# Kernel tuning notes

Hardware: AMD Instinct MI355X
Metric: run time of the kernel (lower is better)

## Reference

```python
import jax, jax.numpy as jnp
import numpy as np

N, T, I, H = 64, 256, 512, 1024


def mish(x):
    return x * jnp.tanh(jax.nn.softplus(x))


def setup_inputs() -> dict:
    key = jax.random.key(0)
    ks = jax.random.split(key, 10)
    s_i = 1.0 / np.sqrt(I)
    s_h = 1.0 / np.sqrt(H)
    return {
        "x": jax.random.normal(ks[0], (N, T, I), dtype=jnp.float32),
        "is_init": jax.random.randint(ks[1], (N, T), 0, 2) > 0,
        "hx": jax.random.normal(ks[2], (N, T, H), dtype=jnp.float32),
        "cx": jax.random.normal(ks[3], (N, T, H), dtype=jnp.float32),
        "W_ih": jax.random.normal(ks[4], (4 * H, I), dtype=jnp.float32) * s_i,
        "W_hh": jax.random.normal(ks[5], (4 * H, H), dtype=jnp.float32) * s_h,
        "b_ih": jax.random.normal(ks[6], (4 * H,), dtype=jnp.float32) * s_h,
        "b_hh": jax.random.normal(ks[7], (4 * H,), dtype=jnp.float32) * s_h,
        "W_out": jax.random.normal(ks[8], (H, H), dtype=jnp.float32) * s_h,
        "b_out": jax.random.normal(ks[9], (H,), dtype=jnp.float32) * s_h,
    }


def reference(x, is_init, hx, cx, W_ih, W_hh, b_ih, b_hh, W_out, b_out):
    # recurrent_mode branch: scan LSTMCell over time with reset masking
    reset = 1.0 - is_init.astype(x.dtype)[..., None]          # [N,T,1]
    h0, c0 = hx[:, 0], cx[:, 0]                                # [N,H]

    def step(carry, inp):
        h, c = carry
        x_t, r_t = inp                                         # [N,I], [N,1]
        h = h * r_t
        c = c * r_t
        gates = x_t @ W_ih.T + b_ih + h @ W_hh.T + b_hh       # [N,4H]
        i_g, f_g, g_g, o_g = jnp.split(gates, 4, axis=-1)
        c = jax.nn.sigmoid(f_g) * c + jax.nn.sigmoid(i_g) * jnp.tanh(g_g)
        h = jax.nn.sigmoid(o_g) * jnp.tanh(c)
        return (h, c), h

    xs = (jnp.swapaxes(x, 0, 1), jnp.swapaxes(reset, 0, 1))    # time-major
    (h_f, c_f), hs = jax.lax.scan(step, (h0, c0), xs)
    hs = jnp.swapaxes(hs, 0, 1)                                # [N,T,H]
    out = mish(hs @ W_out.T + b_out)                           # Linear + Mish
    t = hs.shape[1]
    return (out,
            jnp.broadcast_to(h_f[:, None, :], (h_f.shape[0], t, h_f.shape[1])),
            jnp.broadcast_to(c_f[:, None, :], (c_f.shape[0], t, c_f.shape[1])))
```

## Files before the change

### kernel.cpp

```cpp
#include <hip/hip_runtime.h>
#include <math.h>

#define N_ 64
#define T_ 256
#define I_ 512
#define H_ 1024

typedef unsigned short u16;
typedef unsigned int u32;
typedef unsigned long long u64;
typedef short bf16x8 __attribute__((ext_vector_type(8)));
typedef float f32x4 __attribute__((ext_vector_type(4)));
typedef u16 u16x4 __attribute__((ext_vector_type(4)));

__device__ __forceinline__ u16 f2bf(float f) {
    union { float f; unsigned int u; } x; x.f = f;
    unsigned int r = (x.u + 0x7FFFu + ((x.u >> 16) & 1u)) >> 16;
    return (u16)r;
}
__device__ __forceinline__ float bf2f(u16 u) {
    union { unsigned int u; float f; } x; x.u = ((unsigned int)u) << 16;
    return x.f;
}
__device__ __forceinline__ float sigf(float v) {
    return 1.0f / (1.0f + __expf(-v));
}
__device__ __forceinline__ float tanhfast(float x) {
    float e = __expf(2.0f * x);
    return 1.0f - 2.0f / (e + 1.0f);
}

__device__ __forceinline__ void gload_lds16n(const void* g, void* l) {
    __builtin_amdgcn_global_load_lds(
        (__attribute__((address_space(1))) void*)(g),
        (__attribute__((address_space(3))) void*)(l), 16, 0, 0);
}

#define VMW(Ncnt) do { \
    asm volatile("s_waitcnt vmcnt(" #Ncnt ")" ::: "memory"); \
    __builtin_amdgcn_sched_barrier(0); } while (0)

__device__ __forceinline__ float* c_ptr(int n, int t, int j, float* cA, float* cB) {
    return (n < 32) ? (cA + (((size_t)(n * 256 + t)) << 10) + j)
                    : (cB + (((size_t)((n - 32) * 256 + t)) << 10) + j);
}


__global__ __launch_bounds__(256) void pack_weights(
    const float* __restrict__ W_ih, const float* __restrict__ W_hh,
    const float* __restrict__ b_ih, const float* __restrict__ b_hh,
    u16* __restrict__ Wp, float* __restrict__ bp)
{
    const int rp = blockIdx.x;
    const int j = rp >> 2, g = rp & 3;
    const int src = g * H_ + j;
    const float* wi = W_ih + (size_t)src * I_;
    const float* wh = W_hh + (size_t)src * H_;
    u16* dst = Wp + (size_t)rp * (I_ + H_);
    for (int k = threadIdx.x; k < I_; k += 256) dst[k] = f2bf(wi[k]);
    for (int k = threadIdx.x; k < H_; k += 256) dst[I_ + k] = f2bf(wh[k]);
    if (threadIdx.x == 0) bp[rp] = b_ih[src] + b_hh[src];
}

__global__ __launch_bounds__(256) void conv_x(
    const float* __restrict__ x, u16* __restrict__ x_tb)
{
    const int t = blockIdx.x, n = blockIdx.y;
    const float* s = x + ((size_t)n * T_ + t) * I_;
    u16* d = x_tb + ((size_t)t * N_ + n) * I_;
    for (int k = threadIdx.x; k < I_; k += 256) d[k] = f2bf(s[k]);
}

__global__ __launch_bounds__(256) void conv_wout(
    const float* __restrict__ W, u16* __restrict__ Wb)
{
    const size_t base = (size_t)blockIdx.x * 1024 + threadIdx.x;
    #pragma unroll
    for (int q = 0; q < 4; ++q) Wb[base + q * 256] = f2bf(W[base + q * 256]);
}

__global__ __launch_bounds__(256) void conv_hx(
    const float* __restrict__ hx, u16* __restrict__ hxbf)
{
    const int idx = blockIdx.x * 256 + threadIdx.x;
    const int n = idx >> 10, j = idx & (H_ - 1);
    hxbf[idx] = f2bf(hx[(size_t)n * T_ * H_ + j]);
}

__global__ __launch_bounds__(256) void prep_rel(
    const int* __restrict__ is_init, u16* __restrict__ rel16)
{
    __shared__ u16 ii[256];
    const int n = blockIdx.x, t = threadIdx.x;
    ii[t] = (u16)(is_init[n * T_ + t] != 0);
    __syncthreads();
    int rel = t + 1;
    for (int d = 0; d <= t; ++d) {
        if (ii[t - d]) { rel = d; break; }
    }
    rel16[n * T_ + t] = (u16)rel;
}

__global__ __launch_bounds__(256) void prep_bucket(
    const u16* __restrict__ rel16, u16* __restrict__ entries, u32* __restrict__ offs)
{
    __shared__ u32 hist[258];
    __shared__ u32 offsh[258];
    const int g = blockIdx.x, tid = threadIdx.x;
    for (int i = tid; i < 258; i += 256) hist[i] = 0;
    __syncthreads();
    for (int i = tid; i < 4096; i += 256) {
        const int n = g * 16 + (i & 15), t = i >> 4;
        atomicAdd(&hist[rel16[n * T_ + t]], 1u);
    }
    __syncthreads();
    if (tid == 0) {
        u32 acc = 0;
        for (int s = 0; s < 258; ++s) { offsh[s] = acc; acc += hist[s]; }
    }
    __syncthreads();
    for (int i = tid; i < 258; i += 256) {
        offs[g * 258 + i] = offsh[i];
        hist[i] = offsh[i];
    }
    __syncthreads();
    for (int i = tid; i < 4096; i += 256) {
        const int n = g * 16 + (i & 15), t = i >> 4;
        const int rel = rel16[n * T_ + t];
        const u32 slot = atomicAdd(&hist[rel], 1u);
        entries[g * 4096 + slot] = (u16)((t << 6) | n);
    }
}

__global__ __launch_bounds__(512) __attribute__((amdgpu_waves_per_eu(2, 2)))
void xgates_mfma(
    const u16* __restrict__ x_tb,
    const u16* __restrict__ Wp,
    const float* __restrict__ bp,
    u16* __restrict__ Xg)
{
    __shared__ u16 bls[2][8192];
    const int bx = blockIdx.x, by = blockIdx.y;
    const int tid = threadIdx.x;
    const int v = tid >> 6, l = tid & 63;
    const int l15 = l & 15, lh = l >> 4;
    const int rowb = bx * 256 + v * 32;
    const int colb = by * 256;

    const u16* ap0 = x_tb + (size_t)(rowb + l15) * I_ + lh * 8;
    const u16* ap1 = x_tb + (size_t)(rowb + 16 + l15) * I_ + lh * 8;
    const u16* bs0 = Wp + (size_t)(colb + (2 * v) * 16 + l15) * 1536 + lh * 8;
    const u16* bs1 = Wp + (size_t)(colb + (2 * v + 1) * 16 + l15) * 1536 + lh * 8;

    f32x4 acc[2][16];
    #pragma unroll
    for (int m = 0; m < 2; ++m)
        #pragma unroll
        for (int nt = 0; nt < 16; ++nt) acc[m][nt] = f32x4{0.f, 0.f, 0.f, 0.f};

#define STAGEX(S, B) do { \
    gload_lds16n(bs0 + (S) * 32, (char*)bls[B] + (2 * v) * 1024); \
    gload_lds16n(bs1 + (S) * 32, (char*)bls[B] + (2 * v + 1) * 1024); } while (0)

    STAGEX(0, 0);
    VMW(0); __syncthreads();
    int buf = 0;
    for (int s = 0; s < 16; ++s) {
        if (s < 15) STAGEX(s + 1, buf ^ 1);
        bf16x8 a0 = *(const bf16x8*)(ap0 + s * 32);
        bf16x8 a1 = *(const bf16x8*)(ap1 + s * 32);
        const char* bb = (const char*)bls[buf];
        #pragma unroll
        for (int nt = 0; nt < 16; ++nt) {
            bf16x8 bfr = *(const bf16x8*)(bb + nt * 1024 + l * 16);
            acc[0][nt] = __builtin_amdgcn_mfma_f32_16x16x32_bf16(a0, bfr, acc[0][nt], 0, 0, 0);
            acc[1][nt] = __builtin_amdgcn_mfma_f32_16x16x32_bf16(a1, bfr, acc[1][nt], 0, 0, 0);
        }
        VMW(0); __syncthreads();
        buf ^= 1;
    }
#undef STAGEX

    #pragma unroll
    for (int nt = 0; nt < 16; ++nt) {
        const int col = colb + nt * 16 + l15;
        const float bo = bp[col];
        #pragma unroll
        for (int mt = 0; mt < 2; ++mt)
            #pragma unroll
            for (int rg = 0; rg < 4; ++rg) {
                const int row = rowb + mt * 16 + lh * 4 + rg;
                Xg[(size_t)row * 4096 + col] = f2bf(acc[mt][nt][rg] + bo);
            }
    }
}

__global__ __launch_bounds__(256, 1) void lstm_seg(
    const u16* __restrict__ Xg,
    const u16* __restrict__ Wp,
    const float* __restrict__ cx,
    const u16* __restrict__ hxbf,
    const u16* __restrict__ entries,
    const u32* __restrict__ offs,
    u16* __restrict__ hs,
    float* __restrict__ cA,
    float* __restrict__ cB,
    float* __restrict__ c_final,
    u32* __restrict__ flags)
{
    __shared__ u16 wls[65536];
    const int tid = threadIdx.x;
    const int v = tid >> 6, l = tid & 63;
    const int l15 = l & 15, lh = l >> 4;
    const int u = blockIdx.x & 63, g = blockIdx.x >> 6;

    {
        const u16* src = Wp + (size_t)(u * 64 + v * 16 + l15) * 1536 + I_ + lh * 8;
        char* dst = (char*)wls + v * 32768;
        #pragma unroll
        for (int kk = 0; kk < 32; ++kk)
            gload_lds16n(src + kk * 32, dst + kk * 1024);
    }

    const u16* gent = entries + g * 4096;
    const u32* goff = offs + g * 258;
    u32* gflags = flags + g * 64 * 16;
    const char* wlsb = (const char*)wls;

    VMW(0);
    __syncthreads();

    {
        const int m0 = (int)goff[1];
        const int gtid = u * 256 + tid;
        for (int cell = gtid; cell < m0 * 512; cell += 64 * 256) {
            const int ri = cell >> 9, jj = cell & 511;
            const int j = jj * 2;
            const u16 e = gent[ri];
            const int t = e >> 6, n = e & 63;
            const u16* xp = Xg + ((size_t)t * 64 + n) * 4096 + 4 * j;
            const u16x4 xa = *(const u16x4*)(xp);
            const u16x4 xb = *(const u16x4*)(xp + 4);
            const float c0 = sigf(bf2f(xa[0])) * tanhfast(bf2f(xa[2]));
            const float h0 = sigf(bf2f(xa[3])) * tanhfast(c0);
            const float c1 = sigf(bf2f(xb[0])) * tanhfast(bf2f(xb[2]));
            const float h1 = sigf(bf2f(xb[3])) * tanhfast(c1);
            const size_t hrow = ((size_t)n * 256 + t) * 1024;
            __hip_atomic_store((u32*)(hs + hrow + j),
                               (u32)f2bf(h0) | ((u32)f2bf(h1) << 16),
                               __ATOMIC_RELAXED, __HIP_MEMORY_SCOPE_AGENT);
            __hip_atomic_store((u32*)c_ptr(n, t, j, cA, cB), __float_as_uint(c0),
                               __ATOMIC_RELAXED, __HIP_MEMORY_SCOPE_AGENT);
            __hip_atomic_store((u32*)c_ptr(n, t, j + 1, cA, cB), __float_as_uint(c1),
                               __ATOMIC_RELAXED, __HIP_MEMORY_SCOPE_AGENT);
            if (t == T_ - 1) {
                c_final[n * H_ + j] = c0;
                c_final[n * H_ + j + 1] = c1;
            }
        }
    }
    VMW(0);
    __syncthreads();
    if (tid == 0)
        __hip_atomic_store(gflags + u * 16, 1u,
                           __ATOMIC_RELAXED, __HIP_MEMORY_SCOPE_AGENT);
    if (tid < 64) {
        while (__hip_atomic_load(gflags + tid * 16, __ATOMIC_RELAXED,
                                 __HIP_MEMORY_SCOPE_AGENT) < 1u)
            __builtin_amdgcn_s_sleep(1);
    }
    __syncthreads();
    __builtin_amdgcn_sched_barrier(0);

    for (int s = 1; s <= 256; ++s) {
        if (goff[s] >= 4096u) break;
        const int base = (int)goff[s];
        const int last = (int)goff[s + 1] - 1;
        const int ntiles = ((last + 1 - base) + 15) >> 4;

        for (int mt = v; mt < ntiles; mt += 4) {
            const int ridx = base + mt * 16 + l15;
            const bool valid = (ridx <= last);
            const u16 e = gent[valid ? ridx : last];
            const int t = e >> 6, n = e & 63;

            const u16* rowsrc = (t == 0) ? (hxbf + n * 1024)
                               : (hs + ((size_t)n * 256 + (t - 1)) * 1024);
            const char* lsrc = (const char*)rowsrc + lh * 16;
            bf16x8 a[32];
            #pragma unroll
            for (int kk = 0; kk < 32; ++kk)
                a[kk] = *(const bf16x8*)(lsrc + kk * 64);

            const u16* xrow = Xg + ((size_t)t * 64 + n) * 4096;
            u16x4 xg[4]; float cprev[4];
            #pragma unroll
            for (int q = 0; q < 4; ++q) {
                const int jbq = u * 16 + q * 4 + lh;
                xg[q] = *(const u16x4*)(xrow + 4 * jbq);
                const float* cp = (t == 0) ? (cx + (size_t)n * T_ * H_ + jbq)
                                           : c_ptr(n, t - 1, jbq, cA, cB);
                cprev[q] = *cp;
            }

            f32x4 acc[4];
            #pragma unroll
            for (int q = 0; q < 4; ++q) acc[q] = f32x4{0.f, 0.f, 0.f, 0.f};
            #pragma unroll
            for (int q = 0; q < 4; ++q) {
                #pragma unroll
                for (int kk = 0; kk < 32; ++kk) {
                    bf16x8 wf = *(const bf16x8*)(wlsb + q * 32768 + kk * 1024 + l * 16);
                    acc[q] = __builtin_amdgcn_mfma_f32_16x16x32_bf16(wf, a[kk], acc[q], 0, 0, 0);
                }
            }

            #pragma unroll
            for (int q = 0; q < 4; ++q) {
                const int jbq = u * 16 + q * 4 + lh;
                const float ig = acc[q][0] + bf2f(xg[q][0]);
                const float fg = acc[q][1] + bf2f(xg[q][1]);
                const float gg = acc[q][2] + bf2f(xg[q][2]);
                const float og = acc[q][3] + bf2f(xg[q][3]);
                const float cn = sigf(fg) * cprev[q] + sigf(ig) * tanhfast(gg);
                const float hv = sigf(og) * tanhfast(cn);

                const float hvp = __shfl_down(hv, 16);
                if (valid && !(lh & 1)) {
                    __hip_atomic_store((u32*)(hs + ((size_t)n * 256 + t) * 1024 + jbq),
                                       (u32)f2bf(hv) | ((u32)f2bf(hvp) << 16),
                                       __ATOMIC_RELAXED, __HIP_MEMORY_SCOPE_AGENT);
                }
                if (valid) {
                    __hip_atomic_store((u32*)c_ptr(n, t, jbq, cA, cB),
                                       __float_as_uint(cn),
                                       __ATOMIC_RELAXED, __HIP_MEMORY_SCOPE_AGENT);
                    if (t == T_ - 1) c_final[n * H_ + jbq] = cn;
                }
            }
        }

        VMW(0);
        __syncthreads();
        if (tid == 0)
            __hip_atomic_store(gflags + u * 16, (u32)(s + 1),
                               __ATOMIC_RELAXED, __HIP_MEMORY_SCOPE_AGENT);
        if (tid < 64) {
            while (__hip_atomic_load(gflags + tid * 16, __ATOMIC_RELAXED,
                                     __HIP_MEMORY_SCOPE_AGENT) < (u32)(s + 1))
                __builtin_amdgcn_s_sleep(1);
        }
        __syncthreads();
        __builtin_amdgcn_sched_barrier(0);
    }
}

__global__ __launch_bounds__(512) __attribute__((amdgpu_waves_per_eu(2, 2)))
void out_proj_mfma(
    const u16* __restrict__ hs,
    const u16* __restrict__ Wo,
    const float* __restrict__ b_out,
    float* __restrict__ out0)
{
    __shared__ u16 bls[2][8192];
    const int bx = blockIdx.x, by = blockIdx.y;
    const int tid = threadIdx.x;
    const int v = tid >> 6, l = tid & 63;
    const int l15 = l & 15, lh = l >> 4;
    const int rowb = bx * 256 + v * 32;
    const int colb = by * 256;

    const u16* ap0 = hs + (size_t)(rowb + l15) * H_ + lh * 8;
    const u16* ap1 = hs + (size_t)(rowb + 16 + l15) * H_ + lh * 8;
    const u16* bs0 = Wo + (size_t)(colb + (2 * v) * 16 + l15) * H_ + lh * 8;
    const u16* bs1 = Wo + (size_t)(colb + (2 * v + 1) * 16 + l15) * H_ + lh * 8;

    f32x4 acc[2][16];
    #pragma unroll
    for (int m = 0; m < 2; ++m)
        #pragma unroll
        for (int nt = 0; nt < 16; ++nt) acc[m][nt] = f32x4{0.f, 0.f, 0.f, 0.f};

#define STAGEO(S, B) do { \
    gload_lds16n(bs0 + (S) * 32, (char*)bls[B] + (2 * v) * 1024); \
    gload_lds16n(bs1 + (S) * 32, (char*)bls[B] + (2 * v + 1) * 1024); } while (0)

    STAGEO(0, 0);
    VMW(0); __syncthreads();
    int buf = 0;
    for (int s = 0; s < 32; ++s) {
        if (s < 31) STAGEO(s + 1, buf ^ 1);
        bf16x8 a0 = *(const bf16x8*)(ap0 + s * 32);
        bf16x8 a1 = *(const bf16x8*)(ap1 + s * 32);
        const char* bb = (const char*)bls[buf];
        #pragma unroll
        for (int nt = 0; nt < 16; ++nt) {
            bf16x8 bfr = *(const bf16x8*)(bb + nt * 1024 + l * 16);
            acc[0][nt] = __builtin_amdgcn_mfma_f32_16x16x32_bf16(a0, bfr, acc[0][nt], 0, 0, 0);
            acc[1][nt] = __builtin_amdgcn_mfma_f32_16x16x32_bf16(a1, bfr, acc[1][nt], 0, 0, 0);
        }
        VMW(0); __syncthreads();
        buf ^= 1;
    }
#undef STAGEO

    #pragma unroll
    for (int nt = 0; nt < 16; ++nt) {
        const int col = colb + nt * 16 + l15;
        const float bo = b_out[col];
        #pragma unroll
        for (int mt = 0; mt < 2; ++mt)
            #pragma unroll
            for (int rg = 0; rg < 4; ++rg) {
                const int row = rowb + mt * 16 + lh * 4 + rg;
                const float y = acc[mt][nt][rg] + bo;
                const float sp = (y > 15.f) ? y : log1pf(__expf(y));
                out0[(size_t)row * H_ + col] = y * tanhfast(sp);
            }
    }
}

__global__ __launch_bounds__(256) void bcast_h(
    const u16* __restrict__ hs, float* __restrict__ out1)
{
    const size_t total = (size_t)N_ * T_ * H_;
    for (size_t idx = (size_t)blockIdx.x * 256 + threadIdx.x; idx < total;
         idx += (size_t)gridDim.x * 256) {
        const int n = (int)(idx >> 18);
        const int j = (int)(idx & (H_ - 1));
        out1[idx] = bf2f(hs[((size_t)n * T_ + (T_ - 1)) * H_ + j]);
    }
}

__global__ __launch_bounds__(256) void bcast_c(
    const float* __restrict__ c_final, float* __restrict__ out2)
{
    const size_t total = (size_t)N_ * T_ * H_;
    for (size_t idx = (size_t)blockIdx.x * 256 + threadIdx.x; idx < total;
         idx += (size_t)gridDim.x * 256) {
        const int n = (int)(idx >> 18);
        const int j = (int)(idx & (H_ - 1));
        out2[idx] = c_final[n * H_ + j];
    }
}

extern "C" void kernel_launch(void* const* d_in, const int* in_sizes, int n_in,
                              void* d_out, int out_size, void* d_ws, size_t ws_size,
                              hipStream_t stream) {
    const float* x      = (const float*)d_in[0];
    const int*   is_ini = (const int*)  d_in[1];
    const float* hx     = (const float*)d_in[2];
    const float* cx     = (const float*)d_in[3];
    const float* W_ih   = (const float*)d_in[4];
    const float* W_hh   = (const float*)d_in[5];
    const float* b_ih   = (const float*)d_in[6];
    const float* b_hh   = (const float*)d_in[7];
    const float* W_out  = (const float*)d_in[8];
    const float* b_out  = (const float*)d_in[9];

    float* out0 = (float*)d_out;
    float* out1 = out0 + (size_t)N_ * T_ * H_;
    float* out2 = out1 + (size_t)N_ * T_ * H_;

    char* ws = (char*)d_ws;
    u16*   x_tb    = (u16*)  (ws + 0);
    u16*   Wp      = (u16*)  (ws + 16777216);
    float* bp      = (float*)(ws + 29360128);
    u16*   Wo_b    = (u16*)  (ws + 29376512);
    float* c_final = (float*)(ws + 31473664);
    u16*   hxbf    = (u16*)  (ws + 31735808);
    u16*   rel16   = (u16*)  (ws + 31866880);
    u16*   entries = (u16*)  (ws + 31899648);
    u32*   offs    = (u32*)  (ws + 31932416);
    u32*   flags   = (u32*)  (ws + 31945472);
    float* cB      = (float*)(ws + 31961856);

    u16*   Xg = (u16*)out0;
    u16*   hs = (u16*)out2;
    float* cA = (float*)(out2 + (size_t)32 * 256 * 1024);

    hipMemsetAsync(flags, 0, 16384, stream);
    pack_weights<<<4096, 256, 0, stream>>>(W_ih, W_hh, b_ih, b_hh, Wp, bp);
    conv_x<<<dim3(T_, N_), 256, 0, stream>>>(x, x_tb);
    conv_wout<<<1024, 256, 0, stream>>>(W_out, Wo_b);
    conv_hx<<<256, 256, 0, stream>>>(hx, hxbf);
    prep_rel<<<64, 256, 0, stream>>>(is_ini, rel16);
    prep_bucket<<<4, 256, 0, stream>>>(rel16, entries, offs);

    xgates_mfma<<<dim3(64, 16), 512, 0, stream>>>(x_tb, Wp, bp, Xg);

    lstm_seg<<<256, 256, 0, stream>>>(Xg, Wp, cx, hxbf, entries, offs,
                                      hs, cA, cB, c_final, flags);

    out_proj_mfma<<<dim3(64, 4), 512, 0, stream>>>(hs, Wo_b, b_out, out0);
    bcast_h<<<2048, 256, 0, stream>>>(hs, out1);
    bcast_c<<<2048, 256, 0, stream>>>(c_final, out2);
}
```

Baseline: 1.067 ms.

## Permute gate rows for vectorized h/c stores and double-buffer tile loads

Reorders packed weight rows so that each lane owns four consecutive hidden units. This lets h be written as one 64-bit bf16x4 store and c as two 64-bit stores, with no cross-lane shuffle. The per-step tile loop is also software-pipelined with two register buffers, so the next tile's h-row, x-gate and c-prev loads are issued before the current tile's MFMAs. Risks are doubled register pressure from two 32-entry bf16x8 arrays, which could spill or reduce occupancy, and the need for the permutation to stay consistent with the Xg layout.

```diff
diff --git a/kernel.cpp b/kernel.cpp
--- a/kernel.cpp
+++ b/kernel.cpp
@@ -52,8 +52,10 @@
     u16* __restrict__ Wp, float* __restrict__ bp)
 {
     const int rp = blockIdx.x;
-    const int j = rp >> 2, g = rp & 3;
-    const int src = g * H_ + j;
+    const int g = rp & 3, jp = rp >> 2;
+    const int loc = jp & 15;
+    const int jsrc = (jp & ~15) + ((loc & 3) << 2) + (loc >> 2);
+    const int src = g * H_ + jsrc;
     const float* wi = W_ih + (size_t)src * I_;
     const float* wh = W_hh + (size_t)src * H_;
     u16* dst = Wp + (size_t)rp * (I_ + H_);
@@ -235,28 +237,26 @@
         const int gtid = u * 256 + tid;
         for (int cell = gtid; cell < m0 * 512; cell += 64 * 256) {
             const int ri = cell >> 9, jj = cell & 511;
-            const int j = jj * 2;
+            const int jt = jj * 2;
             const u16 e = gent[ri];
             const int t = e >> 6, n = e & 63;
-            const u16* xp = Xg + ((size_t)t * 64 + n) * 4096 + 4 * j;
-            const u16x4 xa = *(const u16x4*)(xp);
-            const u16x4 xb = *(const u16x4*)(xp + 4);
+            const int loc = jt & 15;
+            const int jp = (jt & ~15) + ((loc & 3) << 2) + (loc >> 2);
+            const u16* xrow = Xg + ((size_t)t * 64 + n) * 4096;
+            const u16x4 xa = *(const u16x4*)(xrow + 4 * jp);
+            const u16x4 xb = *(const u16x4*)(xrow + 4 * jp + 16);
             const float c0 = sigf(bf2f(xa[0])) * tanhfast(bf2f(xa[2]));
             const float h0 = sigf(bf2f(xa[3])) * tanhfast(c0);
             const float c1 = sigf(bf2f(xb[0])) * tanhfast(bf2f(xb[2]));
             const float h1 = sigf(bf2f(xb[3])) * tanhfast(c1);
             const size_t hrow = ((size_t)n * 256 + t) * 1024;
-            __hip_atomic_store((u32*)(hs + hrow + j),
+            __hip_atomic_store((u32*)(hs + hrow + jt),
                                (u32)f2bf(h0) | ((u32)f2bf(h1) << 16),
                                __ATOMIC_RELAXED, __HIP_MEMORY_SCOPE_AGENT);
-            __hip_atomic_store((u32*)c_ptr(n, t, j, cA, cB), __float_as_uint(c0),
+            const u64 cpk = (u64)__float_as_uint(c0) | ((u64)__float_as_uint(c1) << 32);
+            __hip_atomic_store((u64*)c_ptr(n, t, jt, cA, cB), cpk,
                                __ATOMIC_RELAXED, __HIP_MEMORY_SCOPE_AGENT);
-            __hip_atomic_store((u32*)c_ptr(n, t, j + 1, cA, cB), __float_as_uint(c1),
-                               __ATOMIC_RELAXED, __HIP_MEMORY_SCOPE_AGENT);
-            if (t == T_ - 1) {
-                c_final[n * H_ + j] = c0;
-                c_final[n * H_ + j + 1] = c1;
-            }
+            if (t == T_ - 1) *(float2*)(c_final + n * H_ + jt) = float2{c0, c1};
         }
     }
     VMW(0);
@@ -272,71 +272,91 @@
     __syncthreads();
     __builtin_amdgcn_sched_barrier(0);
 
+    bf16x8 Aa[32], Ba[32];
+    u16x4 Axg[4], Bxg[4];
+    float Acp[4], Bcp[4];
+    int At = 0, An = 0, Bt = 0, Bn = 0;
+    bool Av = false, Bv = false;
+
+#define LOADT(P, MT) do { \
+    const int ridx_ = base + (MT) * 16 + l15; \
+    P##v = (ridx_ <= last); \
+    const u16 e_ = gent[P##v ? ridx_ : last]; \
+    P##t = e_ >> 6; P##n = e_ & 63; \
+    const u16* rowsrc_ = (P##t == 0) ? (hxbf + P##n * 1024) \
+                       : (hs + ((size_t)P##n * 256 + (P##t - 1)) * 1024); \
+    const char* lsrc_ = (const char*)rowsrc_ + lh * 16; \
+    _Pragma("unroll") \
+    for (int kk_ = 0; kk_ < 32; ++kk_) \
+        P##a[kk_] = *(const bf16x8*)(lsrc_ + kk_ * 64); \
+    const u16* xrow_ = Xg + ((size_t)P##t * 64 + P##n) * 4096; \
+    _Pragma("unroll") \
+    for (int q_ = 0; q_ < 4; ++q_) { \
+        P##xg[q_] = *(const u16x4*)(xrow_ + 4 * (u * 16 + q_ * 4 + lh)); \
+        const int jt_ = u * 16 + lh * 4 + q_; \
+        P##cp[q_] = (P##t == 0) ? cx[(size_t)P##n * T_ * H_ + jt_] \
+                                : *c_ptr(P##n, P##t - 1, jt_, cA, cB); \
+    } \
+} while (0)
+
+#define PROCT(P) do { \
+    f32x4 acc_[4]; \
+    _Pragma("unroll") \
+    for (int q_ = 0; q_ < 4; ++q_) acc_[q_] = f32x4{0.f, 0.f, 0.f, 0.f}; \
+    _Pragma("unroll") \
+    for (int q_ = 0; q_ < 4; ++q_) { \
+        _Pragma("unroll") \
+        for (int kk_ = 0; kk_ < 32; ++kk_) { \
+            bf16x8 wf_ = *(const bf16x8*)(wlsb + q_ * 32768 + kk_ * 1024 + l * 16); \
+            acc_[q_] = __builtin_amdgcn_mfma_f32_16x16x32_bf16(wf_, P##a[kk_], acc_[q_], 0, 0, 0); \
+        } \
+    } \
+    float cn_[4], hv_[4]; \
+    _Pragma("unroll") \
+    for (int q_ = 0; q_ < 4; ++q_) { \
+        const float ig_ = acc_[q_][0] + bf2f(P##xg[q_][0]); \
+        const float fg_ = acc_[q_][1] + bf2f(P##xg[q_][1]); \
+        const float gg_ = acc_[q_][2] + bf2f(P##xg[q_][2]); \
+        const float og_ = acc_[q_][3] + bf2f(P##xg[q_][3]); \
+        cn_[q_] = sigf(fg_) * P##cp[q_] + sigf(ig_) * tanhfast(gg_); \
+        hv_[q_] = sigf(og_) * tanhfast(cn_[q_]); \
+    } \
+    if (P##v) { \
+        const int jt0_ = u * 16 + lh * 4; \
+        const u64 hp_ = (u64)f2bf(hv_[0]) | ((u64)f2bf(hv_[1]) << 16) \
+                      | ((u64)f2bf(hv_[2]) << 32) | ((u64)f2bf(hv_[3]) << 48); \
+        __hip_atomic_store((u64*)(hs + ((size_t)P##n * 256 + P##t) * 1024 + jt0_), \
+                           hp_, __ATOMIC_RELAXED, __HIP_MEMORY_SCOPE_AGENT); \
+        float* cp0_ = c_ptr(P##n, P##t, jt0_, cA, cB); \
+        const u64 c01_ = (u64)__float_as_uint(cn_[0]) | ((u64)__float_as_uint(cn_[1]) << 32); \
+        const u64 c23_ = (u64)__float_as_uint(cn_[2]) | ((u64)__float_as_uint(cn_[3]) << 32); \
+        __hip_atomic_store((u64*)cp0_, c01_, __ATOMIC_RELAXED, __HIP_MEMORY_SCOPE_AGENT); \
+        __hip_atomic_store((u64*)(cp0_ + 2), c23_, __ATOMIC_RELAXED, __HIP_MEMORY_SCOPE_AGENT); \
+        if (P##t == T_ - 1) \
+            *(float4*)(c_final + P##n * H_ + jt0_) = float4{cn_[0], cn_[1], cn_[2], cn_[3]}; \
+    } \
+} while (0)
+
     for (int s = 1; s <= 256; ++s) {
         if (goff[s] >= 4096u) break;
         const int base = (int)goff[s];
         const int last = (int)goff[s + 1] - 1;
         const int ntiles = ((last + 1 - base) + 15) >> 4;
 
-        for (int mt = v; mt < ntiles; mt += 4) {
-            const int ridx = base + mt * 16 + l15;
-            const bool valid = (ridx <= last);
-            const u16 e = gent[valid ? ridx : last];
-            const int t = e >> 6, n = e & 63;
-
-            const u16* rowsrc = (t == 0) ? (hxbf + n * 1024)
-                               : (hs + ((size_t)n * 256 + (t - 1)) * 1024);
-            const char* lsrc = (const char*)rowsrc + lh * 16;
-            bf16x8 a[32];
-            #pragma unroll
-            for (int kk = 0; kk < 32; ++kk)
-                a[kk] = *(const bf16x8*)(lsrc + kk * 64);
-
-            const u16* xrow = Xg + ((size_t)t * 64 + n) * 4096;
-            u16x4 xg[4]; float cprev[4];
-            #pragma unroll
-            for (int q = 0; q < 4; ++q) {
-                const int jbq = u * 16 + q * 4 + lh;
-                xg[q] = *(const u16x4*)(xrow + 4 * jbq);
-                const float* cp = (t == 0) ? (cx + (size_t)n * T_ * H_ + jbq)
-                                           : c_ptr(n, t - 1, jbq, cA, cB);
-                cprev[q] = *cp;
-            }
-
-            f32x4 acc[4];
-            #pragma unroll
-            for (int q = 0; q < 4; ++q) acc[q] = f32x4{0.f, 0.f, 0.f, 0.f};
-            #pragma unroll
-            for (int q = 0; q < 4; ++q) {
-                #pragma unroll
-                for (int kk = 0; kk < 32; ++kk) {
-                    bf16x8 wf = *(const bf16x8*)(wlsb + q * 32768 + kk * 1024 + l * 16);
-                    acc[q] = __builtin_amdgcn_mfma_f32_16x16x32_bf16(wf, a[kk], acc[q], 0, 0, 0);
-                }
-            }
-
-            #pragma unroll
-            for (int q = 0; q < 4; ++q) {
-                const int jbq = u * 16 + q * 4 + lh;
-                const float ig = acc[q][0] + bf2f(xg[q][0]);
-                const float fg = acc[q][1] + bf2f(xg[q][1]);
-                const float gg = acc[q][2] + bf2f(xg[q][2]);
-                const float og = acc[q][3] + bf2f(xg[q][3]);
-                const float cn = sigf(fg) * cprev[q] + sigf(ig) * tanhfast(gg);
-                const float hv = sigf(og) * tanhfast(cn);
-
-                const float hvp = __shfl_down(hv, 16);
-                if (valid && !(lh & 1)) {
-                    __hip_atomic_store((u32*)(hs + ((size_t)n * 256 + t) * 1024 + jbq),
-                                       (u32)f2bf(hv) | ((u32)f2bf(hvp) << 16),
-                                       __ATOMIC_RELAXED, __HIP_MEMORY_SCOPE_AGENT);
-                }
-                if (valid) {
-                    __hip_atomic_store((u32*)c_ptr(n, t, jbq, cA, cB),
-                                       __float_as_uint(cn),
-                                       __ATOMIC_RELAXED, __HIP_MEMORY_SCOPE_AGENT);
-                    if (t == T_ - 1) c_final[n * H_ + jbq] = cn;
-                }
+        int mt = v;
+        if (mt < ntiles) {
+            LOADT(A, mt);
+            while (true) {
+                int nx = mt + 4;
+                if (nx < ntiles) LOADT(B, nx);
+                PROCT(A);
+                mt = nx;
+                if (mt >= ntiles) break;
+                nx = mt + 4;
+                if (nx < ntiles) LOADT(A, nx);
+                PROCT(B);
+                mt = nx;
+                if (mt >= ntiles) break;
             }
         }
 
@@ -353,6 +373,8 @@
         __syncthreads();
         __builtin_amdgcn_sched_barrier(0);
     }
+#undef LOADT
+#undef PROCT
 }
 
 __global__ __launch_bounds__(512) __attribute__((amdgpu_waves_per_eu(2, 2)))
```

Result: faster. 1.000 ms (-6.3%).
